# Kernel optimization log

Measured on AMD Instinct MI355X. Metric: run time of the kernel, lower is better.

Reference implementation:

```python
import jax
jax.config.update("jax_enable_x64", True)
import jax.numpy as jnp
import numpy as np

B = 4            # batch size
Z, Y, X = 41, 1024, 1024   # spatial shape (all coords < 1025, matching the hash base)
NT = 2_000_000   # raw teacher voxels (with duplicates)
NS = 800_000     # student voxels (subset of teacher unique coords)
C = 32           # feature channels
M = 1025         # hash base from the original module


def _hash(idx):
    # idx: [N,4] int -> int64 scalar hash; batch in high bits so sorting the hash
    # == lexicographic sort by (batch, c1, c2, c3), matching torch.unique(dim=0).
    w = jnp.array([M ** 3, M ** 2, M, 1], dtype=jnp.int64)
    return idx.astype(jnp.int64) @ w


def setup_inputs() -> dict:
    rng = np.random.default_rng(0)
    b = rng.integers(0, B, NT)
    z = rng.integers(0, Z, NT)
    y = rng.integers(0, Y, NT)
    x = rng.integers(0, X, NT)
    teacher_indices = np.stack([b, z, y, x], axis=1).astype(np.int32)

    # student indices must be a subset of teacher's unique coords (forward asserts this)
    h = (b.astype(np.int64) * M ** 3 + z.astype(np.int64) * M ** 2
         + y.astype(np.int64) * M + x.astype(np.int64))
    _, first = np.unique(h, return_index=True)
    pick = rng.choice(first, size=NS, replace=False)
    student_indices = teacher_indices[pick]

    key = jax.random.key(0)
    teacher_features = jax.random.normal(key, (NT, C), dtype=jnp.float32)
    return {
        "teacher_features": teacher_features,
        "teacher_indices": jnp.asarray(teacher_indices),
        "student_indices": jnp.asarray(student_indices),
    }


def reference(teacher_features, teacher_indices, student_indices):
    n_t = teacher_indices.shape[0]
    FILL = jnp.int64(2 ** 62)  # padding hash, sorts to the end

    # --- bev_out_3d: unique(dim=0) + index_add_ dedup ---
    h_t = _hash(teacher_indices)
    uniq, first_idx, inv = jnp.unique(
        h_t, size=n_t, fill_value=FILL, return_index=True, return_inverse=True
    )
    feat_unique = jax.ops.segment_sum(teacher_features, inv, num_segments=n_t)

    # --- per-batch isin join + masked gather ---
    # Teacher unique rows are hash-sorted (== lex-sorted by batch, coords).
    # The matched subset, in teacher order, is exactly the sorted student hashes
    # (student is a subset of teacher unique), concatenated batch-by-batch ==
    # a single global sort since batch occupies the high bits.
    h_s = jnp.sort(_hash(student_indices))
    pos = jnp.searchsorted(uniq, h_s)          # [NS] positions into unique rows
    feat = feat_unique[pos]                    # [NS, C]
    indice = teacher_indices[first_idx[pos]]   # [NS, 4]
    return feat, indice
```

## Files before the change

### kernel.cpp

```cpp
#include <hip/hip_runtime.h>
#include <stdint.h>

typedef unsigned long long u64;
typedef u64 u64x2 __attribute__((ext_vector_type(2)));

#define NWORDS 2686976u
#define GW 4096u
#define NGROUPS 656u

struct __align__(16) Combo { u64 word; uint32_t prefix; uint32_t pad; };

__device__ __forceinline__ uint32_t pack4(int4 v) {
    return (((uint32_t)v.x * 41u + (uint32_t)v.y) << 20) |
           ((uint32_t)v.z << 10) | (uint32_t)v.w;
}

__global__ void set_bits(const int* __restrict__ sidx, Combo* __restrict__ combo, int ns) {
    int i = blockIdx.x * blockDim.x + threadIdx.x;
    if (i >= ns) return;
    uint32_t k = pack4(((const int4*)sidx)[i]);
    atomicOr(&combo[k >> 6].word, 1ull << (k & 63u));
}

__global__ void group_popcount(const Combo* __restrict__ combo, uint32_t* __restrict__ groupSum) {
    __shared__ uint32_t s[256];
    uint32_t t = 0;
    size_t base = (size_t)blockIdx.x * GW;
    #pragma unroll
    for (int j = 0; j < 16; ++j)
        t += (uint32_t)__popcll(combo[base + j * 256u + threadIdx.x].word);
    s[threadIdx.x] = t;
    __syncthreads();
    #pragma unroll
    for (int off = 128; off > 0; off >>= 1) {
        if (threadIdx.x < (unsigned)off) s[threadIdx.x] += s[threadIdx.x + off];
        __syncthreads();
    }
    if (threadIdx.x == 0) groupSum[blockIdx.x] = s[0];
}

__global__ void word_prefix_indice(Combo* __restrict__ combo,
                                   const uint32_t* __restrict__ groupSum,
                                   float* __restrict__ outI) {
    __shared__ uint32_t s[256];
    __shared__ uint32_t baseSh;
    const int tid = threadIdx.x, bid = blockIdx.x;
    size_t w0 = (size_t)bid * GW + (size_t)tid * 16;
    u64 w[16];
    uint32_t tsum = 0;
    #pragma unroll
    for (int j = 0; j < 16; ++j) { w[j] = combo[w0 + j].word; tsum += (uint32_t)__popcll(w[j]); }
    s[tid] = tsum;
    __syncthreads();
    #pragma unroll
    for (int off = 1; off < 256; off <<= 1) {
        uint32_t u = (tid >= off) ? s[tid - off] : 0u;
        __syncthreads();
        s[tid] += u;
        __syncthreads();
    }
    uint32_t exclInBlock = s[tid] - tsum;
    if (tid < 64) {
        uint32_t sum = 0;
        for (int g = tid; g < bid; g += 64) sum += groupSum[g];
        #pragma unroll
        for (int off = 32; off > 0; off >>= 1) sum += __shfl_down(sum, off);
        if (tid == 0) baseSh = sum;
    }
    __syncthreads();
    uint32_t run = baseSh + exclInBlock;
    #pragma unroll
    for (int j = 0; j < 16; ++j) {
        u64x2 rec; rec.x = w[j]; rec.y = (u64)run;
        ((u64x2*)combo)[w0 + j] = rec;
        u64 word = w[j];
        uint32_t kw = (uint32_t)(w0 + j) << 6;
        while (word) {
            int b = (int)__builtin_ctzll(word);
            word &= word - 1;
            uint32_t k = kw | (uint32_t)b;
            uint32_t bz = k >> 20;
            ((float4*)outI)[run++] = make_float4(
                (float)(bz / 41u), (float)(bz % 41u),
                (float)((k >> 10) & 1023u), (float)(k & 1023u));
        }
    }
}

__global__ void teacher_fused(const int* __restrict__ tidx, const float* __restrict__ tfeat,
                              const Combo* __restrict__ combo, uint32_t* __restrict__ cnt,
                              uint2* __restrict__ ovf, uint32_t* __restrict__ ovfCount,
                              float* __restrict__ feat, int nt) {
    int t = blockIdx.x * blockDim.x + threadIdx.x;
    if (t >= nt) return;
    uint32_t k = pack4(((const int4*)tidx)[t]);
    u64x2 e = ((const u64x2*)combo)[k >> 6];
    u64 word = e.x;
    u64 bit  = 1ull << (k & 63u);
    if (!(word & bit)) return;
    int p = (int)((uint32_t)e.y + (uint32_t)__popcll(word & (bit - 1ull)));
    uint32_t old = atomicAdd(&cnt[p], 1u);
    if (old == 0u) {
        const float4* src = (const float4*)(tfeat + (size_t)t * 32);
        float4* dst = (float4*)(feat + (size_t)p * 32);
        #pragma unroll
        for (int q = 0; q < 8; ++q) dst[q] = src[q];
    } else {
        uint32_t idx = atomicAdd(ovfCount, 1u);
        ovf[idx] = make_uint2((uint32_t)t, (uint32_t)p);
    }
}

__global__ void drain_ovf(const float* __restrict__ tfeat, const uint2* __restrict__ ovf,
                          const uint32_t* __restrict__ ovfCount, float* __restrict__ feat) {
    uint32_t n = *ovfCount;
    for (uint32_t i = blockIdx.x * blockDim.x + threadIdx.x; i < n;
         i += gridDim.x * blockDim.x) {
        uint2 e = ovf[i];
        const float4* src = (const float4*)(tfeat + (size_t)e.x * 32);
        float* dst = feat + (size_t)e.y * 32;
        #pragma unroll
        for (int q = 0; q < 8; ++q) {
            float4 f = src[q];
            atomicAdd(dst + q * 4 + 0, f.x);
            atomicAdd(dst + q * 4 + 1, f.y);
            atomicAdd(dst + q * 4 + 2, f.z);
            atomicAdd(dst + q * 4 + 3, f.w);
        }
    }
}

extern "C" void kernel_launch(void* const* d_in, const int* in_sizes, int n_in,
                              void* d_out, int out_size, void* d_ws, size_t ws_size,
                              hipStream_t stream) {
    const float* tfeat = (const float*)d_in[0];
    const int*   tidx  = (const int*)d_in[1];
    const int*   sidx  = (const int*)d_in[2];

    const int NT = in_sizes[1] / 4;
    const int NS = in_sizes[2] / 4;

    float* feat = (float*)d_out;
    float* outI = (float*)d_out + (size_t)NS * 32;

    char* base = (char*)d_ws;
    Combo*    combo    = (Combo*)base;
    uint32_t* cnt      = (uint32_t*)(base + (size_t)NWORDS * sizeof(Combo));
    uint32_t* ovfCount = cnt + NS;
    size_t    zeroBytes = (size_t)NWORDS * sizeof(Combo) + (size_t)NS * 4 + 8;
    uint32_t* groupSum = ovfCount + 2;
    uint2*    ovf      = (uint2*)(groupSum + NGROUPS);

    hipMemsetAsync(d_ws, 0, zeroBytes, stream);

    set_bits<<<(NS + 255) / 256, 256, 0, stream>>>(sidx, combo, NS);
    group_popcount<<<NGROUPS, 256, 0, stream>>>(combo, groupSum);
    word_prefix_indice<<<NGROUPS, 256, 0, stream>>>(combo, groupSum, outI);
    teacher_fused<<<(NT + 255) / 256, 256, 0, stream>>>(tidx, tfeat, combo, cnt,
                                                        ovf, ovfCount, feat, NT);
    drain_ovf<<<512, 256, 0, stream>>>(tfeat, ovf, ovfCount, feat);
}
```

Measured before the change: 226.2 us.

## Split interleaved bitmap+prefix struct into separate word and prefix arrays

Replaces the 16-byte interleaved {word, prefix} record with a dense u64 bitmap and a separate uint32 prefix array. The memset, atomicOr, popcount and prefix scan then touch half as many bytes in the bitmap, and the prefix write is 4 bytes instead of a 16-byte record. The cost is that teacher lookups now issue two scattered loads instead of one 16-byte load. Teacher feature loads are also hoisted ahead of the atomic so they can overlap with it, which adds register pressure.

```diff
diff --git a/kernel.cpp b/kernel.cpp
--- a/kernel.cpp
+++ b/kernel.cpp
@@ -2,33 +2,30 @@
 #include <stdint.h>
 
 typedef unsigned long long u64;
-typedef u64 u64x2 __attribute__((ext_vector_type(2)));
 
 #define NWORDS 2686976u
 #define GW 4096u
 #define NGROUPS 656u
-
-struct __align__(16) Combo { u64 word; uint32_t prefix; uint32_t pad; };
 
 __device__ __forceinline__ uint32_t pack4(int4 v) {
     return (((uint32_t)v.x * 41u + (uint32_t)v.y) << 20) |
            ((uint32_t)v.z << 10) | (uint32_t)v.w;
 }
 
-__global__ void set_bits(const int* __restrict__ sidx, Combo* __restrict__ combo, int ns) {
+__global__ void set_bits(const int* __restrict__ sidx, u64* __restrict__ words, int ns) {
     int i = blockIdx.x * blockDim.x + threadIdx.x;
     if (i >= ns) return;
     uint32_t k = pack4(((const int4*)sidx)[i]);
-    atomicOr(&combo[k >> 6].word, 1ull << (k & 63u));
+    atomicOr(&words[k >> 6], 1ull << (k & 63u));
 }
 
-__global__ void group_popcount(const Combo* __restrict__ combo, uint32_t* __restrict__ groupSum) {
+__global__ void group_popcount(const u64* __restrict__ words, uint32_t* __restrict__ groupSum) {
     __shared__ uint32_t s[256];
     uint32_t t = 0;
     size_t base = (size_t)blockIdx.x * GW;
     #pragma unroll
     for (int j = 0; j < 16; ++j)
-        t += (uint32_t)__popcll(combo[base + j * 256u + threadIdx.x].word);
+        t += (uint32_t)__popcll(words[base + j * 256u + threadIdx.x]);
     s[threadIdx.x] = t;
     __syncthreads();
     #pragma unroll
@@ -39,8 +36,9 @@
     if (threadIdx.x == 0) groupSum[blockIdx.x] = s[0];
 }
 
-__global__ void word_prefix_indice(Combo* __restrict__ combo,
+__global__ void word_prefix_indice(const u64* __restrict__ words,
                                    const uint32_t* __restrict__ groupSum,
+                                   uint32_t* __restrict__ prefixArr,
                                    float* __restrict__ outI) {
     __shared__ uint32_t s[256];
     __shared__ uint32_t baseSh;
@@ -49,7 +47,7 @@
     u64 w[16];
     uint32_t tsum = 0;
     #pragma unroll
-    for (int j = 0; j < 16; ++j) { w[j] = combo[w0 + j].word; tsum += (uint32_t)__popcll(w[j]); }
+    for (int j = 0; j < 16; ++j) { w[j] = words[w0 + j]; tsum += (uint32_t)__popcll(w[j]); }
     s[tid] = tsum;
     __syncthreads();
     #pragma unroll
@@ -71,8 +69,7 @@
     uint32_t run = baseSh + exclInBlock;
     #pragma unroll
     for (int j = 0; j < 16; ++j) {
-        u64x2 rec; rec.x = w[j]; rec.y = (u64)run;
-        ((u64x2*)combo)[w0 + j] = rec;
+        prefixArr[w0 + j] = run;
         u64 word = w[j];
         uint32_t kw = (uint32_t)(w0 + j) << 6;
         while (word) {
@@ -88,23 +85,26 @@
 }
 
 __global__ void teacher_fused(const int* __restrict__ tidx, const float* __restrict__ tfeat,
-                              const Combo* __restrict__ combo, uint32_t* __restrict__ cnt,
+                              const u64* __restrict__ words, const uint32_t* __restrict__ prefixArr,
+                              uint32_t* __restrict__ cnt,
                               uint2* __restrict__ ovf, uint32_t* __restrict__ ovfCount,
                               float* __restrict__ feat, int nt) {
     int t = blockIdx.x * blockDim.x + threadIdx.x;
     if (t >= nt) return;
     uint32_t k = pack4(((const int4*)tidx)[t]);
-    u64x2 e = ((const u64x2*)combo)[k >> 6];
-    u64 word = e.x;
-    u64 bit  = 1ull << (k & 63u);
+    u64 word = words[k >> 6];
+    uint32_t pfx = prefixArr[k >> 6];
+    u64 bit = 1ull << (k & 63u);
     if (!(word & bit)) return;
-    int p = (int)((uint32_t)e.y + (uint32_t)__popcll(word & (bit - 1ull)));
+    int p = (int)(pfx + (uint32_t)__popcll(word & (bit - 1ull)));
+    const float4* src = (const float4*)(tfeat + (size_t)t * 32);
+    float4 f0 = src[0], f1 = src[1], f2 = src[2], f3 = src[3];
+    float4 f4 = src[4], f5 = src[5], f6 = src[6], f7 = src[7];
     uint32_t old = atomicAdd(&cnt[p], 1u);
     if (old == 0u) {
-        const float4* src = (const float4*)(tfeat + (size_t)t * 32);
         float4* dst = (float4*)(feat + (size_t)p * 32);
-        #pragma unroll
-        for (int q = 0; q < 8; ++q) dst[q] = src[q];
+        dst[0] = f0; dst[1] = f1; dst[2] = f2; dst[3] = f3;
+        dst[4] = f4; dst[5] = f5; dst[6] = f6; dst[7] = f7;
     } else {
         uint32_t idx = atomicAdd(ovfCount, 1u);
         ovf[idx] = make_uint2((uint32_t)t, (uint32_t)p);
@@ -144,19 +144,20 @@
     float* outI = (float*)d_out + (size_t)NS * 32;
 
     char* base = (char*)d_ws;
-    Combo*    combo    = (Combo*)base;
-    uint32_t* cnt      = (uint32_t*)(base + (size_t)NWORDS * sizeof(Combo));
+    u64*      words    = (u64*)base;
+    uint32_t* cnt      = (uint32_t*)(base + (size_t)NWORDS * 8);
     uint32_t* ovfCount = cnt + NS;
-    size_t    zeroBytes = (size_t)NWORDS * sizeof(Combo) + (size_t)NS * 4 + 8;
-    uint32_t* groupSum = ovfCount + 2;
-    uint2*    ovf      = (uint2*)(groupSum + NGROUPS);
+    size_t    zeroBytes = (size_t)NWORDS * 8 + (size_t)NS * 4 + 8;
+    uint32_t* groupSum  = ovfCount + 2;
+    uint32_t* prefixArr = groupSum + NGROUPS;
+    uint2*    ovf       = (uint2*)(prefixArr + NWORDS);
 
     hipMemsetAsync(d_ws, 0, zeroBytes, stream);
 
-    set_bits<<<(NS + 255) / 256, 256, 0, stream>>>(sidx, combo, NS);
-    group_popcount<<<NGROUPS, 256, 0, stream>>>(combo, groupSum);
-    word_prefix_indice<<<NGROUPS, 256, 0, stream>>>(combo, groupSum, outI);
-    teacher_fused<<<(NT + 255) / 256, 256, 0, stream>>>(tidx, tfeat, combo, cnt,
+    set_bits<<<(NS + 255) / 256, 256, 0, stream>>>(sidx, words, NS);
+    group_popcount<<<NGROUPS, 256, 0, stream>>>(words, groupSum);
+    word_prefix_indice<<<NGROUPS, 256, 0, stream>>>(words, groupSum, prefixArr, outI);
+    teacher_fused<<<(NT + 255) / 256, 256, 0, stream>>>(tidx, tfeat, words, prefixArr, cnt,
                                                         ovf, ovfCount, feat, NT);
     drain_ovf<<<512, 256, 0, stream>>>(tfeat, ovf, ovfCount, feat);
 }
```

Measured after the change: 212.7 us. 1.06x faster.
